# Kernel tuning notes

Hardware: AMD Instinct MI355X
Metric: run time of the kernel (lower is better)

The kernel has to match this reference:

```python
import jax, jax.numpy as jnp
import numpy as np

N, C_IN, T, V = 64, 64, 64, 25
C_OUT = 64
DK = DV = 16
NH = 8
DKH, DVH = DK // NH, DV // NH
KT = 9
EPS = 1e-5


def make_pe(channel, joint_num, time_len):
    # temporal positional encoding: position index = frame id, repeated per joint
    pos = np.repeat(np.arange(time_len), joint_num).astype(np.float32)[:, None]
    pe = np.zeros((time_len * joint_num, channel), np.float32)
    div = np.exp(np.arange(0, channel, 2).astype(np.float32) * -(np.log(10000.0) / channel))
    pe[:, 0::2] = np.sin(pos * div)
    pe[:, 1::2] = np.cos(pos * div)
    return jnp.asarray(pe.reshape(time_len, joint_num, channel).transpose(2, 0, 1)[None])  # (1,C,time,joint)


def setup_inputs():
    key = jax.random.key(0)
    ks = jax.random.split(key, 17)
    rn = lambda k, s, sc=0.05: jax.random.normal(k, s, jnp.float32) * sc
    return {
        'x': jax.random.normal(ks[0], (N, C_IN, T, V), jnp.float32),
        'pe': make_pe(C_IN, V, 64),
        'data_bn_g': 1.0 + rn(ks[1], (C_IN * V,)),
        'data_bn_b': rn(ks[2], (C_IN * V,)),
        'qkv_w': rn(ks[3], (3 * DK + DV, C_IN), 0.1),
        'qkv_b': rn(ks[4], (3 * DK + DV,)),
        'attn_w': rn(ks[5], (DV, DV), 0.1),
        'attn_b': rn(ks[6], (DV,)),
        'tcn_w': rn(ks[7], (C_OUT - DV, C_IN, KT, 1), 0.05),
        'tcn_b': rn(ks[8], (C_OUT - DV,)),
        'tcn_bn_g': 1.0 + rn(ks[9], (C_OUT - DV,)),
        'tcn_bn_b': rn(ks[10], (C_OUT - DV,)),
        'fc1_w': rn(ks[11], (C_OUT // 2, C_OUT), 0.1),
        'fc1_b': rn(ks[12], (C_OUT // 2,)),
        'fc2_w': rn(ks[13], (C_OUT, C_OUT // 2), 0.1),
        'fc2_b': rn(ks[14], (C_OUT,)),
        'bn_g': 1.0 + rn(ks[15], (C_OUT,)),
        'bn_b': rn(ks[16], (C_OUT,)),
    }


def _bn_eval(x, g, b, axis=1):
    # eval-mode BatchNorm with running_mean=0, running_var=1
    shape = [1] * x.ndim
    shape[axis] = -1
    scale = g / jnp.sqrt(1.0 + EPS)
    return x * scale.reshape(shape) + b.reshape(shape)


def _qkv_heads(x2d, qkv_w, qkv_b):
    # x2d: (B, C, T); 1x1 conv == channel matmul; split q/k/g/v, g is projected but unused
    qkv = jnp.einsum('oc,bct->bot', qkv_w, x2d) + qkv_b[None, :, None]
    q, k, _g, v = jnp.split(qkv, [DK, 2 * DK, 3 * DK], axis=1)
    B = x2d.shape[0]
    split = lambda z, ch: z.reshape(B, NH, ch // NH, -1)  # (B, Nh, chh, T)
    q = split(q, DK) * (DKH ** -0.5)
    return q, split(k, DK), split(v, DV)


def reference(x, pe, data_bn_g, data_bn_b, qkv_w, qkv_b, attn_w, attn_b,
              tcn_w, tcn_b, tcn_bn_g, tcn_bn_b, fc1_w, fc1_b, fc2_w, fc2_b, bn_g, bn_b):
    y = x + pe[:, :, :T]                                 # positional encoding (N,C,T,V)
    x_sum = x
    # data_bn over flattened (C*V) channels
    xb = x.transpose(0, 1, 3, 2).reshape(N, C_IN * V, T)
    xb = _bn_eval(xb, data_bn_g, data_bn_b)
    xn = xb.reshape(N, C_IN, V, T).transpose(0, 1, 3, 2)  # (N,C,T,V)
    # fold joints into batch: (N*V, C, T)
    xf = xn.transpose(0, 3, 1, 2).reshape(N * V, C_IN, T)
    yf = y.transpose(0, 3, 1, 2).reshape(N * V, C_IN, T)
    fq, fk, fv = _qkv_heads(xf, qkv_w, qkv_b)
    pq, pk, _ = _qkv_heads(yf, qkv_w, qkv_b)
    mu_q = fq.mean(-1, keepdims=True)                     # (B,H,dkh,1)
    fqc = fq - mu_q
    logits_pos = jnp.einsum('bhcs,bhct->bhst', pq, pk)    # (B,H,T,T)
    pairwise = jnp.einsum('bhcs,bhct->bhst', fqc, fk)     # (B,H,T,T)
    unary = jnp.einsum('bhcs,bhct->bhst', mu_q, fk)       # (B,H,1,T)
    weights = jnp.tanh(pairwise + logits_pos) + jnp.tanh(unary + logits_pos)
    ao = jnp.einsum('bhst,bhct->bhsc', weights, fv)       # (B,H,T,dvh)
    # (B,H,1,T,dvh) -> permute(0,1,4,2,3) -> combine heads -> (B, DV, T)
    ao = ao.transpose(0, 1, 3, 2).reshape(N * V, DV, T)
    ao = jnp.einsum('oc,bct->bot', attn_w, ao) + attn_b[None, :, None]
    ao = ao.reshape(N, V, DV, T).transpose(0, 2, 3, 1)    # (N, DV, T, V)
    # temporal conv branch (Unit2D: conv(k=9 temporal) + eval BN)
    tc = jax.lax.conv_general_dilated(x_sum, tcn_w, (1, 1), ((KT // 2, KT // 2), (0, 0)),
                                      dimension_numbers=('NCHW', 'OIHW', 'NCHW'))
    tc = tc + tcn_b[None, :, None, None]
    tc = _bn_eval(tc, tcn_bn_g, tcn_bn_b)
    result = jnp.concatenate([tc, ao], axis=1) + x_sum    # residual (down is None)
    # SE-style channel gating
    se = result.mean(axis=(2, 3))                         # (N, C_OUT)
    gate = jax.nn.sigmoid(jax.nn.relu(se @ fc1_w.T + fc1_b) @ fc2_w.T + fc2_b)
    result = result * gate[:, :, None, None] + result
    result = _bn_eval(result, bn_g, bn_b)
    return jax.nn.relu(result)
```

## Files before the change

kernel.cpp:

```cpp
#include <hip/hip_runtime.h>
#include <hip/hip_bf16.h>
#include <math.h>

#define TV_ 1600
#define SCALE_K 2.885390081777927f
#define RS2_ 0.70710678118654752f

typedef __attribute__((ext_vector_type(8))) short bf16x8;
typedef __attribute__((ext_vector_type(4))) float f32x4;
typedef __attribute__((ext_vector_type(2))) __fp16 h2f;

union F4H { float4 f; h2f h[4]; };
union F2H { float2 f; h2f h[2]; };

__device__ __forceinline__ float tanh4(float y) {
    float e = __builtin_amdgcn_exp2f(y);
    float r = __builtin_amdgcn_rcpf(e + 1.f);
    return __builtin_fmaf(-2.f, r, 1.f);
}

__device__ __forceinline__ float dot2f(h2f a, h2f b, float c) {
    return __builtin_amdgcn_fdot2(a, b, c, false);
}

__device__ __forceinline__ ushort f2bf(float f) {
    __hip_bfloat16 h = __float2bfloat16(f);
    return *(ushort*)&h;
}
__device__ __forceinline__ float bf2f(ushort u) {
    uint w = ((uint)u) << 16;
    return __uint_as_float(w);
}

__global__ __launch_bounds__(256) void t1_kernel(
    const float* __restrict__ x, const float* __restrict__ pe,
    const float* __restrict__ tcn_w, const float* __restrict__ tg,
    const float* __restrict__ qkv_w, const float* __restrict__ qkv_b,
    ushort* __restrict__ rt, float* __restrict__ Sp, float* __restrict__ Tt,
    ushort* __restrict__ wb, ushort* __restrict__ wq, float* __restrict__ qb,
    ushort* __restrict__ pet)
{
    const int tid = threadIdx.x;
    const int bx = blockIdx.x, by = blockIdx.y;

    if (bx == 25) {
        #pragma unroll 1
        for (int j = 0; j < 9; ++j) {
            int idx = by * 256 + tid + j * 16384;
            if (idx < 27648) {
                int oc = idx / 576, kk = idx - oc * 576;
                int kt = kk >> 6, ci = kk & 63;
                float a = tg[oc] * rsqrtf(1.f + 1e-5f);
                wb[idx] = f2bf(tcn_w[(oc * 64 + ci) * 9 + kt] * a);
            } else if (idx < 32768) {
                int i2 = idx - 27648;
                int r = i2 >> 6, c = i2 & 63;
                int src; float sc;
                if (r < 16)      { src = r;      sc = RS2_; }
                else if (r < 32) { src = r;      sc = SCALE_K; }
                else if (r < 48) { src = r + 16; sc = 1.f; }
                else if (r < 64) { src = r - 48; sc = RS2_; }
                else             { src = r - 48; sc = SCALE_K; }
                wq[i2] = f2bf(qkv_w[src * 64 + c] * sc);
            } else if (idx < 32848) {
                int r = idx - 32768;
                int src; float sc;
                if (r < 16)      { src = r;      sc = RS2_; }
                else if (r < 32) { src = r;      sc = SCALE_K; }
                else if (r < 48) { src = r + 16; sc = 1.f; }
                else if (r < 64) { src = r - 48; sc = RS2_; }
                else             { src = r - 48; sc = SCALE_K; }
                qb[r] = qkv_b[src] * sc;
            } else if (idx < 135248) {
                int i3 = idx - 32848;
                int ci = i3 / 1600, tv = i3 - ci * 1600;
                pet[tv * 64 + ci] = f2bf(pe[ci * 1600 + tv]);
            }
        }
        return;
    }
    if (bx == 26) {
        const int n = by;
        #pragma unroll
        for (int it = 0; it < 2; ++it) {
            int item = tid + it * 256;
            int ci = item >> 3, slot = item & 7;
            int t = (slot < 4) ? slot : (56 + slot);
            const float* xp = x + (n * 64 + ci) * TV_ + t * 25;
            float s = 0.f;
            #pragma unroll
            for (int v = 0; v < 25; ++v) s += xp[v];
            Tt[(n * 64 + ci) * 8 + slot] = s;
        }
        return;
    }

    __shared__ ushort smt[64 * 66];
    __shared__ float sps[64 * 65];
    const int tv0 = bx * 64;
    const int n = by;
    const int tvl = tid & 63, cig = tid >> 6;
    const int tv = tv0 + tvl;

    #pragma unroll
    for (int k = 0; k < 16; ++k) {
        int ci = cig * 16 + k;
        float xv = x[(n * 64 + ci) * TV_ + tv];
        smt[tvl * 66 + ci] = f2bf(xv);
        sps[ci * 65 + tvl] = xv;
    }
    __syncthreads();

    {
        const int c = tid >> 2, qr = tid & 3;
        float s = 0.f;
        #pragma unroll
        for (int i = 0; i < 16; ++i) s += sps[c * 65 + qr * 16 + i];
        s += __shfl_xor(s, 1);
        s += __shfl_xor(s, 2);
        if (qr == 0) Sp[(n * 25 + bx) * 64 + c] = s;
    }

    #pragma unroll
    for (int j = 0; j < 8; ++j) {
        int chunk = tid + j * 256;
        int tvr = chunk >> 5, p = chunk & 31;
        uint val = *(const uint*)&smt[tvr * 66 + p * 2];
        *(uint*)&rt[(n * TV_ + tv0 + tvr) * 64 + p * 2] = val;
    }
}

__global__ __launch_bounds__(256, 5) void score_kernel(
    const ushort* __restrict__ rt, const ushort* __restrict__ pet,
    const float* __restrict__ dbg, const float* __restrict__ dbb,
    const ushort* __restrict__ wq, const float* __restrict__ qb,
    const float* __restrict__ attn_w, const float* __restrict__ attn_b,
    float* __restrict__ aoc, float* __restrict__ sep)
{
    __shared__ float sm[5312];
    ushort* smu = (ushort*)sm;
    const int MU_ = 1056;
    const int FK2 = 1120, PK2 = 1664, FV2 = 2208, PQ2 = 2752, FQ2 = 3296;
    const int AO2 = 3840;

    const int b = blockIdx.x;
    const int l = b >> 3;
    const int n = (b & 7) * 8 + l / 25;
    const int v = l % 25;
    const int tid = threadIdx.x;

    const int lane = tid & 63, wave = tid >> 6;
    const int m16 = lane & 15, q = lane >> 4;

    {
        const int part = tid & 7;
        const int ci0 = part * 8;
        const float rs = rsqrtf(1.f + 1e-5f);
        float sc8[8], sh8[8];
        #pragma unroll
        for (int i = 0; i < 8; ++i) {
            sc8[i] = dbg[(ci0 + i) * 25 + v] * rs;
            sh8[i] = dbb[(ci0 + i) * 25 + v];
        }
        #pragma unroll
        for (int j = 0; j < 2; ++j) {
            int t = (tid + j * 256) >> 3;
            uint4 xr = *(const uint4*)&rt[(n * TV_ + t * 25 + v) * 64 + ci0];
            uint4 pr = *(const uint4*)&pet[(t * 25 + v) * 64 + ci0];
            const ushort* xu = (const ushort*)&xr;
            const ushort* pu = (const ushort*)&pr;
            ushort xs[8], ys[8];
            #pragma unroll
            for (int i = 0; i < 8; ++i) {
                float xf = bf2f(xu[i]);
                xs[i] = f2bf(xf * sc8[i] + sh8[i]);
                ys[i] = f2bf(xf + bf2f(pu[i]));
            }
            *(uint4*)&smu[t * 72 + ci0] = *(uint4*)xs;
            *(uint4*)&smu[4608 + t * 72 + ci0] = *(uint4*)ys;
        }
    }
    __syncthreads();

    f32x4 acc[5];
    #pragma unroll
    for (int mt = 0; mt < 5; ++mt) acc[mt] = (f32x4){0.f, 0.f, 0.f, 0.f};
    #pragma unroll
    for (int kt = 0; kt < 2; ++kt) {
        const int koff = kt * 32 + q * 8;
        bf16x8 bx = *(const bf16x8*)&smu[(wave * 16 + m16) * 72 + koff];
        bf16x8 by = *(const bf16x8*)&smu[4608 + (wave * 16 + m16) * 72 + koff];
        #pragma unroll
        for (int mt = 0; mt < 5; ++mt) {
            bf16x8 a = *(const bf16x8*)&wq[(mt * 16 + m16) * 64 + koff];
            acc[mt] = __builtin_amdgcn_mfma_f32_16x16x32_bf16(a, (mt < 3) ? bx : by, acc[mt], 0, 0, 0);
        }
    }
    __syncthreads();

    {
        const int t = wave * 16 + m16;
        #pragma unroll
        for (int r = 0; r < 4; ++r)
            sm[(q * 4 + r) * 66 + t] = acc[0][r] + qb[q * 4 + r];
        const int p0 = (2 * q) * 68 + t, p1 = (2 * q + 1) * 68 + t;
        *(h2f*)&sm[FK2 + p0] = __builtin_amdgcn_cvt_pkrtz(acc[1][0] + qb[16 + 4 * q],     acc[1][1] + qb[16 + 4 * q + 1]);
        *(h2f*)&sm[FK2 + p1] = __builtin_amdgcn_cvt_pkrtz(acc[1][2] + qb[16 + 4 * q + 2], acc[1][3] + qb[16 + 4 * q + 3]);
        *(h2f*)&sm[FV2 + p0] = __builtin_amdgcn_cvt_pkrtz(acc[2][0] + qb[32 + 4 * q],     acc[2][1] + qb[32 + 4 * q + 1]);
        *(h2f*)&sm[FV2 + p1] = __builtin_amdgcn_cvt_pkrtz(acc[2][2] + qb[32 + 4 * q + 2], acc[2][3] + qb[32 + 4 * q + 3]);
        *(h2f*)&sm[PQ2 + p0] = __builtin_amdgcn_cvt_pkrtz(acc[3][0] + qb[48 + 4 * q],     acc[3][1] + qb[48 + 4 * q + 1]);
        *(h2f*)&sm[PQ2 + p1] = __builtin_amdgcn_cvt_pkrtz(acc[3][2] + qb[48 + 4 * q + 2], acc[3][3] + qb[48 + 4 * q + 3]);
        *(h2f*)&sm[PK2 + p0] = __builtin_amdgcn_cvt_pkrtz(acc[4][0] + qb[64 + 4 * q],     acc[4][1] + qb[64 + 4 * q + 1]);
        *(h2f*)&sm[PK2 + p1] = __builtin_amdgcn_cvt_pkrtz(acc[4][2] + qb[64 + 4 * q + 2], acc[4][3] + qb[64 + 4 * q + 3]);
    }
    __syncthreads();

    if (tid < 64) {
        int ch = tid & 15, qq = tid >> 4;
        float s = 0.f;
        #pragma unroll
        for (int t = 0; t < 16; ++t) s += sm[ch * 66 + qq * 16 + t];
        sm[MU_ + qq * 16 + ch] = s;
    }
    __syncthreads();
    if (tid < 16) {
        float mval = (sm[MU_ + tid] + sm[MU_ + 16 + tid] + sm[MU_ + 32 + tid] + sm[MU_ + 48 + tid]) * (1.f / 64.f);
        sm[MU_ + tid] = mval;
    }
    __syncthreads();

    #pragma unroll
    for (int e = 0; e < 2; ++e) {
        int idx = tid * 2 + e;
        int s = idx >> 3, h = idx & 7;
        float a = sm[(2 * h) * 66 + s] - sm[MU_ + 2 * h];
        float c = sm[(2 * h + 1) * 66 + s] - sm[MU_ + 2 * h + 1];
        *(h2f*)&sm[FQ2 + h * 68 + s] = __builtin_amdgcn_cvt_pkrtz(a, c);
    }
    __syncthreads();

    const int g3 = tid & 7, m3 = tid >> 3;
    const int tb0 = 8 * g3;
    #pragma unroll 1
    for (int h = 0; h < 8; ++h) {
        const int hb = h * 68;
        h2f mupk = __builtin_amdgcn_cvt_pkrtz(sm[MU_ + 2 * h], sm[MU_ + 2 * h + 1]);
        F2H fq2u, pq2u;
        fq2u.f = *(const float2*)&sm[FQ2 + hb + 2 * m3];
        pq2u.f = *(const float2*)&sm[PQ2 + hb + 2 * m3];
        float ao00 = 0.f, ao01 = 0.f, ao10 = 0.f, ao11 = 0.f;
        #pragma unroll
        for (int ch = 0; ch < 2; ++ch) {
            const int base = hb + tb0 + 4 * ch;
            F4H fk4, pk4, fv4;
            fk4.f = *(const float4*)&sm[FK2 + base];
            pk4.f = *(const float4*)&sm[PK2 + base];
            fv4.f = *(const float4*)&sm[FV2 + base];
            float un[4], fv0[4], fv1[4];
            #pragma unroll
            for (int j = 0; j < 4; ++j) {
                un[j] = dot2f(mupk, fk4.h[j], 0.f);
                fv0[j] = (float)fv4.h[j].x;
                fv1[j] = (float)fv4.h[j].y;
            }
            #pragma unroll
            for (int js = 0; js < 2; ++js) {
                h2f fq1 = fq2u.h[js];
                h2f pq1 = pq2u.h[js];
                #pragma unroll
                for (int j = 0; j < 4; ++j) {
                    float lp = dot2f(pq1, pk4.h[j], 0.f);
                    float a1 = dot2f(fq1, fk4.h[j], lp);
                    float a2 = un[j] + lp;
                    float w = tanh4(a1) + tanh4(a2);
                    if (js == 0) { ao00 = __builtin_fmaf(w, fv0[j], ao00); ao01 = __builtin_fmaf(w, fv1[j], ao01); }
                    else         { ao10 = __builtin_fmaf(w, fv0[j], ao10); ao11 = __builtin_fmaf(w, fv1[j], ao11); }
                }
            }
        }
        #pragma unroll
        for (int off = 1; off <= 4; off <<= 1) {
            ao00 += __shfl_xor(ao00, off);
            ao01 += __shfl_xor(ao01, off);
            ao10 += __shfl_xor(ao10, off);
            ao11 += __shfl_xor(ao11, off);
        }
        if (g3 == 0) {
            sm[AO2 + (2 * m3) * 20 + 2 * h]         = ao00;
            sm[AO2 + (2 * m3) * 20 + 2 * h + 1]     = ao01;
            sm[AO2 + (2 * m3 + 1) * 20 + 2 * h]     = ao10;
            sm[AO2 + (2 * m3 + 1) * 20 + 2 * h + 1] = ao11;
        }
    }
    __syncthreads();

    const int t = tid & 63, oq = tid >> 6;
    float aorow[16];
    #pragma unroll
    for (int i = 0; i < 4; ++i)
        *(float4*)&aorow[i * 4] = *(const float4*)&sm[AO2 + t * 20 + i * 4];
    float* aop = aoc + (n * 25 + v) * 1024;
    #pragma unroll
    for (int j = 0; j < 4; ++j) {
        int o = oq * 4 + j;
        float acc4 = attn_b[o];
        #pragma unroll
        for (int c = 0; c < 16; ++c) acc4 += attn_w[o * 16 + c] * aorow[c];
        aop[o * 64 + t] = acc4;
        float ssum = acc4;
        #pragma unroll
        for (int off = 32; off >= 1; off >>= 1) ssum += __shfl_down(ssum, off, 64);
        if ((tid & 63) == 0) sep[(n * 25 + v) * 16 + o] = ssum;
    }
}

__global__ __launch_bounds__(512, 1) void tcn_mfma_kernel(
    const ushort* __restrict__ rt, const float* __restrict__ x,
    const ushort* __restrict__ wb,
    const float* __restrict__ tcn_b, const float* __restrict__ tg,
    const float* __restrict__ tb,
    const float* __restrict__ sep, const float* __restrict__ Sp,
    const float* __restrict__ Tt, const float* __restrict__ aoc,
    const float* __restrict__ fc1w, const float* __restrict__ fc1b,
    const float* __restrict__ fc2w, const float* __restrict__ fc2b,
    const float* __restrict__ bng, const float* __restrict__ bnb,
    float* __restrict__ out)
{
    __shared__ ushort xsl[600 * 72];
    __shared__ float U[576];
    __shared__ float gpart[432];
    __shared__ float SS[64], seL[64], hid[32], gateL[64];

    const int b = blockIdx.x;
    const int n = b >> 2, tile = b & 3;
    const int t0 = tile * 16;
    const int tid = threadIdx.x;
    const float rsbn = rsqrtf(1.f + 1e-5f);

    const int tvbase = (t0 - 4) * 25;
    for (int idx = tid; idx < 4800; idx += 512) {
        int r = idx >> 3, part = idx & 7;
        int tv = tvbase + r;
        uint4 val = make_uint4(0u, 0u, 0u, 0u);
        if (tv >= 0 && tv < TV_) val = *(const uint4*)&rt[(n * TV_ + tv) * 64 + part * 8];
        *(uint4*)&xsl[r * 72 + part * 8] = val;
    }

    if (tid < 64) {
        float S = 0.f;
        #pragma unroll 1
        for (int j = 0; j < 25; ++j) S += Sp[(n * 25 + j) * 64 + tid];
        SS[tid] = S;
        float T[8];
        #pragma unroll
        for (int j = 0; j < 8; ++j) T[j] = Tt[(n * 64 + tid) * 8 + j];
        U[tid * 9 + 0] = S - (T[4] + T[5] + T[6] + T[7]);
        U[tid * 9 + 1] = S - (T[5] + T[6] + T[7]);
        U[tid * 9 + 2] = S - (T[6] + T[7]);
        U[tid * 9 + 3] = S - T[7];
        U[tid * 9 + 4] = S;
        U[tid * 9 + 5] = S - T[0];
        U[tid * 9 + 6] = S - (T[0] + T[1]);
        U[tid * 9 + 7] = S - (T[0] + T[1] + T[2]);
        U[tid * 9 + 8] = S - (T[0] + T[1] + T[2] + T[3]);
    }
    __syncthreads();
    if (tid < 432) {
        int oc = tid / 9, kt = tid - oc * 9;
        float cs = 0.f;
        #pragma unroll
        for (int cb = 0; cb < 8; ++cb) {
            bf16x8 w8 = *(const bf16x8*)&wb[oc * 576 + kt * 64 + cb * 8];
            #pragma unroll
            for (int i = 0; i < 8; ++i)
                cs += bf2f((ushort)w8[i]) * U[(cb * 8 + i) * 9 + kt];
        }
        gpart[tid] = cs;
    }
    __syncthreads();
    if (tid < 64) {
        if (tid < 48) {
            float cs = 0.f;
            #pragma unroll
            for (int kt = 0; kt < 9; ++kt) cs += gpart[tid * 9 + kt];
            float a = tg[tid] * rsbn;
            float cb_ = tcn_b[tid] * a + tb[tid];
            seL[tid] = (a * cs + 1600.f * cb_ + SS[tid]) * (1.f / 1600.f);
        } else {
            float at = 0.f;
            #pragma unroll 1
            for (int j = 0; j < 25; ++j) at += sep[(n * 25 + j) * 16 + tid - 48];
            seL[tid] = (at + SS[tid]) * (1.f / 1600.f);
        }
    }
    __syncthreads();
    if (tid < 32) {
        float a = fc1b[tid];
        #pragma unroll
        for (int c = 0; c < 64; ++c) a += fc1w[tid * 64 + c] * seL[c];
        hid[tid] = fmaxf(a, 0.f);
    }
    __syncthreads();
    if (tid < 64) {
        float g = fc2b[tid];
        #pragma unroll
        for (int j = 0; j < 32; ++j) g += fc2w[tid * 32 + j] * hid[j];
        gateL[tid] = 1.f / (1.f + __expf(-g));
    }
    __syncthreads();

    const int lane = tid & 63, wave = tid >> 6;
    const int m16 = lane & 15, q = lane >> 4;
    const int nt0 = wave * 3;

    f32x4 acc[3][3];
    f32x4 acc24[3];
    #pragma unroll
    for (int i = 0; i < 3; ++i)
        #pragma unroll
        for (int mt = 0; mt < 3; ++mt)
            acc[i][mt] = (f32x4){0.f, 0.f, 0.f, 0.f};
    #pragma unroll
    for (int mt = 0; mt < 3; ++mt) acc24[mt] = (f32x4){0.f, 0.f, 0.f, 0.f};

    for (int ktile = 0; ktile < 18; ++ktile) {
        const int kt = ktile >> 1;
        const int cib = (ktile & 1) * 32 + q * 8;
        bf16x8 afr[3];
        #pragma unroll
        for (int mt = 0; mt < 3; ++mt)
            afr[mt] = *(const bf16x8*)&wb[(mt * 16 + m16) * 576 + ktile * 32 + q * 8];
        #pragma unroll
        for (int i = 0; i < 3; ++i) {
            int p = (nt0 + i) * 16 + m16;
            bf16x8 bfr = *(const bf16x8*)&xsl[(p + kt * 25) * 72 + cib];
            #pragma unroll
            for (int mt = 0; mt < 3; ++mt)
                acc[i][mt] = __builtin_amdgcn_mfma_f32_16x16x32_bf16(afr[mt], bfr, acc[i][mt], 0, 0, 0);
        }
        if (wave == 0) {
            int p = 24 * 16 + m16;
            bf16x8 bfr = *(const bf16x8*)&xsl[(p + kt * 25) * 72 + cib];
            #pragma unroll
            for (int mt = 0; mt < 3; ++mt)
                acc24[mt] = __builtin_amdgcn_mfma_f32_16x16x32_bf16(afr[mt], bfr, acc24[mt], 0, 0, 0);
        }
    }

    float cb3[3][4], m3_[3][4], bb3[3][4];
    #pragma unroll
    for (int mt = 0; mt < 3; ++mt)
        #pragma unroll
        for (int r = 0; r < 4; ++r) {
            int oc = mt * 16 + q * 4 + r;
            float a = tg[oc] * rsbn;
            cb3[mt][r] = tcn_b[oc] * a + tb[oc];
            m3_[mt][r] = (1.f + gateL[oc]) * (bng[oc] * rsbn);
            bb3[mt][r] = bnb[oc];
        }
    #pragma unroll
    for (int i = 0; i < 3; ++i) {
        int posg = tile * 400 + (nt0 + i) * 16 + m16;
        #pragma unroll
        for (int mt = 0; mt < 3; ++mt) {
            #pragma unroll
            for (int r = 0; r < 4; ++r) {
                int oc = mt * 16 + q * 4 + r;
                float val = acc[i][mt][r] + cb3[mt][r] + x[(n * 64 + oc) * TV_ + posg];
                out[(n * 64 + oc) * TV_ + posg] = fmaxf(val * m3_[mt][r] + bb3[mt][r], 0.f);
            }
        }
    }
    if (wave == 0) {
        int posg = tile * 400 + 24 * 16 + m16;
        #pragma unroll
        for (int mt = 0; mt < 3; ++mt) {
            #pragma unroll
            for (int r = 0; r < 4; ++r) {
                int oc = mt * 16 + q * 4 + r;
                float val = acc24[mt][r] + cb3[mt][r] + x[(n * 64 + oc) * TV_ + posg];
                out[(n * 64 + oc) * TV_ + posg] = fmaxf(val * m3_[mt][r] + bb3[mt][r], 0.f);
            }
        }
    }

    __syncthreads();
    float* ts = (float*)xsl;
    for (int task = tid; task < 1600; task += 512) {
        int v = task >> 6;
        int r = task & 63;
        int o = r >> 2, f = r & 3;
        float4 d = *(const float4*)&aoc[(n * 25 + v) * 1024 + o * 64 + tile * 16 + f * 4];
        float* dst = &ts[v * 257 + o * 16 + f * 4];
        dst[0] = d.x; dst[1] = d.y; dst[2] = d.z; dst[3] = d.w;
    }
    __syncthreads();
    for (int p4 = tid; p4 < 1600; p4 += 512) {
        int o = p4 / 100, r4 = p4 - o * 100;
        int base4 = (n * 64 + 48 + o) * 400 + tile * 100 + r4;
        float4 xr = ((const float4*)x)[base4];
        float4 val;
        #pragma unroll
        for (int e = 0; e < 4; ++e) {
            int pos = r4 * 4 + e;
            int lt = pos / 25, v = pos - lt * 25;
            ((float*)&val)[e] = ts[v * 257 + o * 16 + lt];
        }
        float mm = (1.f + gateL[48 + o]) * (bng[48 + o] * rsbn);
        float bb = bnb[48 + o];
        val.x = fmaxf((val.x + xr.x) * mm + bb, 0.f);
        val.y = fmaxf((val.y + xr.y) * mm + bb, 0.f);
        val.z = fmaxf((val.z + xr.z) * mm + bb, 0.f);
        val.w = fmaxf((val.w + xr.w) * mm + bb, 0.f);
        ((float4*)out)[base4] = val;
    }
}

extern "C" void kernel_launch(void* const* d_in, const int* in_sizes, int n_in,
                              void* d_out, int out_size, void* d_ws, size_t ws_size,
                              hipStream_t stream) {
    const float* x     = (const float*)d_in[0];
    const float* pe    = (const float*)d_in[1];
    const float* dbg   = (const float*)d_in[2];
    const float* dbb   = (const float*)d_in[3];
    const float* qkvw  = (const float*)d_in[4];
    const float* qkvb  = (const float*)d_in[5];
    const float* attnw = (const float*)d_in[6];
    const float* attnb = (const float*)d_in[7];
    const float* tcnw  = (const float*)d_in[8];
    const float* tcnb  = (const float*)d_in[9];
    const float* tcng  = (const float*)d_in[10];
    const float* tcnbb = (const float*)d_in[11];
    const float* fc1w  = (const float*)d_in[12];
    const float* fc1b  = (const float*)d_in[13];
    const float* fc2w  = (const float*)d_in[14];
    const float* fc2b  = (const float*)d_in[15];
    const float* bng   = (const float*)d_in[16];
    const float* bnb   = (const float*)d_in[17];

    float* out  = (float*)d_out;
    float* Sp   = (float*)d_ws;
    float* sep  = Sp + 102400;
    float* Tt   = sep + 25600;
    float* qb   = Tt + 32768;
    float* aoc  = qb + 96;
    ushort* wb  = (ushort*)(aoc + 1638400);
    ushort* wq  = wb + 27648;
    ushort* pet = wq + 5120;
    ushort* rt  = pet + 102400;

    t1_kernel<<<dim3(27, 64), dim3(256), 0, stream>>>(
        x, pe, tcnw, tcng, qkvw, qkvb, rt, Sp, Tt, wb, wq, qb, pet);
    score_kernel<<<dim3(1600), dim3(256), 0, stream>>>(rt, pet, dbg, dbb, wq, qb, attnw, attnb, aoc, sep);
    tcn_mfma_kernel<<<dim3(256), dim3(512), 0, stream>>>(
        rt, x, wb, tcnb, tcng, tcnbb, sep, Sp, Tt, aoc,
        fc1w, fc1b, fc2w, fc2b, bng, bnb, out);
}
```

Baseline: 197.3 us.

## Remap attention loop to one head per thread and precompute unary logits

```diff
diff --git a/kernel.cpp b/kernel.cpp
--- a/kernel.cpp
+++ b/kernel.cpp
@@ -137,11 +137,12 @@
     const float* __restrict__ attn_w, const float* __restrict__ attn_b,
     float* __restrict__ aoc, float* __restrict__ sep)
 {
-    __shared__ float sm[5312];
+    __shared__ float sm[5856];
     ushort* smu = (ushort*)sm;
     const int MU_ = 1056;
     const int FK2 = 1120, PK2 = 1664, FV2 = 2208, PQ2 = 2752, FQ2 = 3296;
     const int AO2 = 3840;
+    const int UN_ = 5312;
 
     const int b = blockIdx.x;
     const int l = b >> 3;
@@ -237,60 +238,49 @@
         float c = sm[(2 * h + 1) * 66 + s] - sm[MU_ + 2 * h + 1];
         *(h2f*)&sm[FQ2 + h * 68 + s] = __builtin_amdgcn_cvt_pkrtz(a, c);
     }
-    __syncthreads();
-
-    const int g3 = tid & 7, m3 = tid >> 3;
-    const int tb0 = 8 * g3;
-    #pragma unroll 1
-    for (int h = 0; h < 8; ++h) {
+    {
+        const int h = tid & 7, tt = tid >> 3;
+        h2f mp = __builtin_amdgcn_cvt_pkrtz(sm[MU_ + 2 * h], sm[MU_ + 2 * h + 1]);
+        sm[UN_ + h * 68 + tt]      = dot2f(mp, *(const h2f*)&sm[FK2 + h * 68 + tt], 0.f);
+        sm[UN_ + h * 68 + tt + 32] = dot2f(mp, *(const h2f*)&sm[FK2 + h * 68 + tt + 32], 0.f);
+    }
+    __syncthreads();
+
+    {
+        const int h = tid & 7, sp = tid >> 3;
         const int hb = h * 68;
-        h2f mupk = __builtin_amdgcn_cvt_pkrtz(sm[MU_ + 2 * h], sm[MU_ + 2 * h + 1]);
-        F2H fq2u, pq2u;
-        fq2u.f = *(const float2*)&sm[FQ2 + hb + 2 * m3];
-        pq2u.f = *(const float2*)&sm[PQ2 + hb + 2 * m3];
+        F2H fqp, pqp;
+        fqp.f = *(const float2*)&sm[FQ2 + hb + 2 * sp];
+        pqp.f = *(const float2*)&sm[PQ2 + hb + 2 * sp];
+        const h2f fq0 = fqp.h[0], fq1 = fqp.h[1];
+        const h2f pq0 = pqp.h[0], pq1 = pqp.h[1];
         float ao00 = 0.f, ao01 = 0.f, ao10 = 0.f, ao11 = 0.f;
-        #pragma unroll
-        for (int ch = 0; ch < 2; ++ch) {
-            const int base = hb + tb0 + 4 * ch;
+        #pragma unroll 2
+        for (int t4 = 0; t4 < 16; ++t4) {
             F4H fk4, pk4, fv4;
-            fk4.f = *(const float4*)&sm[FK2 + base];
-            pk4.f = *(const float4*)&sm[PK2 + base];
-            fv4.f = *(const float4*)&sm[FV2 + base];
-            float un[4], fv0[4], fv1[4];
+            fk4.f = *(const float4*)&sm[FK2 + hb + 4 * t4];
+            pk4.f = *(const float4*)&sm[PK2 + hb + 4 * t4];
+            fv4.f = *(const float4*)&sm[FV2 + hb + 4 * t4];
+            float4 un4 = *(const float4*)&sm[UN_ + hb + 4 * t4];
+            const float* unp = (const float*)&un4;
             #pragma unroll
             for (int j = 0; j < 4; ++j) {
-                un[j] = dot2f(mupk, fk4.h[j], 0.f);
-                fv0[j] = (float)fv4.h[j].x;
-                fv1[j] = (float)fv4.h[j].y;
+                float un = unp[j];
+                float fva = (float)fv4.h[j].x, fvb = (float)fv4.h[j].y;
+                float lp0 = dot2f(pq0, pk4.h[j], 0.f);
+                float a10 = dot2f(fq0, fk4.h[j], lp0);
+                float w0 = tanh4(a10) + tanh4(un + lp0);
+                ao00 = __builtin_fmaf(w0, fva, ao00);
+                ao01 = __builtin_fmaf(w0, fvb, ao01);
+                float lp1 = dot2f(pq1, pk4.h[j], 0.f);
+                float a11 = dot2f(fq1, fk4.h[j], lp1);
+                float w1 = tanh4(a11) + tanh4(un + lp1);
+                ao10 = __builtin_fmaf(w1, fva, ao10);
+                ao11 = __builtin_fmaf(w1, fvb, ao11);
             }
-            #pragma unroll
-            for (int js = 0; js < 2; ++js) {
-                h2f fq1 = fq2u.h[js];
-                h2f pq1 = pq2u.h[js];
-                #pragma unroll
-                for (int j = 0; j < 4; ++j) {
-                    float lp = dot2f(pq1, pk4.h[j], 0.f);
-                    float a1 = dot2f(fq1, fk4.h[j], lp);
-                    float a2 = un[j] + lp;
-                    float w = tanh4(a1) + tanh4(a2);
-                    if (js == 0) { ao00 = __builtin_fmaf(w, fv0[j], ao00); ao01 = __builtin_fmaf(w, fv1[j], ao01); }
-                    else         { ao10 = __builtin_fmaf(w, fv0[j], ao10); ao11 = __builtin_fmaf(w, fv1[j], ao11); }
-                }
-            }
-        }
-        #pragma unroll
-        for (int off = 1; off <= 4; off <<= 1) {
-            ao00 += __shfl_xor(ao00, off);
-            ao01 += __shfl_xor(ao01, off);
-            ao10 += __shfl_xor(ao10, off);
-            ao11 += __shfl_xor(ao11, off);
-        }
-        if (g3 == 0) {
-            sm[AO2 + (2 * m3) * 20 + 2 * h]         = ao00;
-            sm[AO2 + (2 * m3) * 20 + 2 * h + 1]     = ao01;
-            sm[AO2 + (2 * m3 + 1) * 20 + 2 * h]     = ao10;
-            sm[AO2 + (2 * m3 + 1) * 20 + 2 * h + 1] = ao11;
-        }
+        }
+        *(float2*)&sm[AO2 + (2 * sp) * 20 + 2 * h]     = make_float2(ao00, ao01);
+        *(float2*)&sm[AO2 + (2 * sp + 1) * 20 + 2 * h] = make_float2(ao10, ao11);
     }
     __syncthreads();
 
```

After: 192.0 us. 1.03x faster.
